# Kernel optimization log

Measured on AMD Instinct MI355X. Metric: run time of the kernel, lower is better.

## Reference

```python
import jax, jax.numpy as jnp
import numpy as np

N_NODES = 50000
N_EDGES = 300000
F_IN = 11
D = 256


def _gcn_conv(h, src, dst, deg_inv_sqrt, W, b, n):
    """PyG GCNConv: out = D^{-1/2} (A + I) D^{-1/2} (h W) + b.
    src/dst already include self-loops; deg_inv_sqrt precomputed."""
    norm = deg_inv_sqrt[src] * deg_inv_sqrt[dst]          # [E+N]
    hw = h @ W                                            # [N, D]
    msg = hw[src] * norm[:, None]                         # [E+N, D]
    out = jax.ops.segment_sum(msg, dst, num_segments=n)   # [N, D]
    return out + b


def setup_inputs() -> dict:
    key = jax.random.key(0)
    ks = jax.random.split(key, 8)
    x = jax.random.normal(ks[0], (N_NODES, F_IN), dtype=jnp.float32)
    edge_index = jax.random.randint(ks[1], (2, N_EDGES), 0, N_NODES, dtype=jnp.int32)
    s = 0.05
    W_embed = jax.random.normal(ks[2], (F_IN, D), dtype=jnp.float32) * s
    b_embed = jnp.zeros((D,), dtype=jnp.float32)
    W1 = jax.random.normal(ks[3], (D, D), dtype=jnp.float32) * s
    b1 = jnp.zeros((D,), dtype=jnp.float32)
    W2 = jax.random.normal(ks[4], (D, D), dtype=jnp.float32) * s
    b2 = jnp.zeros((D,), dtype=jnp.float32)
    return {"x": x, "edge_index": edge_index, "W_embed": W_embed, "b_embed": b_embed,
            "W1": W1, "b1": b1, "W2": W2, "b2": b2}


def reference(x, edge_index, W_embed, b_embed, W1, b1, W2, b2):
    n = x.shape[0]
    # add self-loops (PyG GCNConv default add_self_loops=True)
    loop = jnp.arange(n, dtype=edge_index.dtype)
    src = jnp.concatenate([edge_index[0], loop])
    dst = jnp.concatenate([edge_index[1], loop])
    # symmetric normalization: deg over target index with unit edge weights
    deg = jax.ops.segment_sum(jnp.ones(src.shape, dtype=x.dtype), dst, num_segments=n)
    deg_inv_sqrt = jnp.where(deg > 0, jax.lax.rsqrt(jnp.maximum(deg, 1e-12)), 0.0)

    h = jax.nn.relu(x @ W_embed + b_embed)                # embed + relu
    h = jax.nn.relu(_gcn_conv(h, src, dst, deg_inv_sqrt, W1, b1, n))
    h = _gcn_conv(h, src, dst, deg_inv_sqrt, W2, b2, n)
    return h
```

## Files before the change

kernel.cpp:

```cpp
#include <hip/hip_runtime.h>

#define N_NODES 50000
#define N_EDGES 300000
#define N_TOT   350000
#define D       256
#define MPAD    50048
#define SCAN_B  196

typedef __attribute__((ext_vector_type(8))) short bf16x8;
typedef __attribute__((ext_vector_type(4))) float f32x4;
typedef __attribute__((ext_vector_type(8))) unsigned short u16x8;

__device__ __forceinline__ float bf2f(unsigned short b) {
    union { unsigned u; float f; } v; v.u = ((unsigned)b) << 16; return v.f;
}
__device__ __forceinline__ unsigned short f2bf(float f) {
    union { float f; unsigned u; } v; v.f = f;
    unsigned u = v.u;
    unsigned r = (u + 0x7FFFu + ((u >> 16) & 1u)) >> 16;
    return (unsigned short)r;
}
__device__ __forceinline__ void g2lds16(const unsigned short* g, unsigned short* l) {
    __builtin_amdgcn_global_load_lds(
        (const __attribute__((address_space(1))) void*)g,
        (__attribute__((address_space(3))) void*)l, 16, 0, 0);
}

__global__ __launch_bounds__(256) void k1_kernel(
        const float* __restrict__ x, const int* __restrict__ ei,
        const float* __restrict__ We, const float* __restrict__ be,
        const float* __restrict__ W1, const float* __restrict__ W2,
        int* __restrict__ cnt,
        unsigned short* __restrict__ Wt1, unsigned short* __restrict__ Wt2,
        unsigned short* __restrict__ hA) {
    int t = threadIdx.x, b = blockIdx.x;
    int tid = b * 256 + t;

    if (tid < N_TOT) {
        int dst = (tid < N_EDGES) ? ei[N_EDGES + tid] : (tid - N_EDGES);
        atomicAdd(&cnt[dst], 1);
    }
    if (tid < 2 * D * D) {
        int wsel = tid >> 16, rem = tid & 65535;
        int tt = rem >> 8, bb = rem & 255;
        const float* W = wsel ? W2 : W1;
        unsigned short* Wt = wsel ? Wt2 : Wt1;
        Wt[bb * D + tt] = f2bf(W[tt * D + bb]);
    }
    float w[11];
    #pragma unroll
    for (int k = 0; k < 11; ++k) w[k] = We[k * D + t];
    float bb = be[t];
    #pragma unroll
    for (int ni = 0; ni < 8; ++ni) {
        int node = b * 8 + ni;
        float acc = 0.f;
        if (node < N_NODES) {
            acc = bb;
            #pragma unroll
            for (int k = 0; k < 11; ++k) acc += x[node * 11 + k] * w[k];
            acc = fmaxf(acc, 0.f);
        }
        hA[(size_t)node * D + t] = f2bf(acc);
    }
}

__global__ __launch_bounds__(256) void k2_kernel(const int* __restrict__ cnt,
                                                 float* __restrict__ dis,
                                                 int* __restrict__ locs,
                                                 int* __restrict__ bsum,
                                                 int* __restrict__ done) {
    __shared__ int ws[4];
    __shared__ int amLast;
    int t = threadIdx.x, lane = t & 63, wv = t >> 6;
    int i = blockIdx.x * 256 + t;
    int v = (i < N_NODES) ? cnt[i] : 0;
    if (i < N_NODES) dis[i] = rsqrtf((float)v);
    int s = v;
    #pragma unroll
    for (int d = 1; d < 64; d <<= 1) {
        int u = __shfl_up(s, d, 64);
        if (lane >= d) s += u;
    }
    if (lane == 63) ws[wv] = s;
    __syncthreads();
    int off = 0;
    #pragma unroll
    for (int k = 0; k < 4; ++k) if (k < wv) off += ws[k];
    s += off;
    if (i < N_NODES) locs[i] = s;

    if (t == 255) {
        bsum[blockIdx.x] = s;
        __threadfence();
        amLast = (atomicAdd(done, 1) == SCAN_B - 1);
    }
    __syncthreads();
    if (amLast) {
        __threadfence();
        int vv = 0;
        if (t < SCAN_B)
            vv = __hip_atomic_load(&bsum[t], __ATOMIC_RELAXED, __HIP_MEMORY_SCOPE_AGENT);
        int ss = vv;
        #pragma unroll
        for (int d = 1; d < 64; d <<= 1) {
            int u = __shfl_up(ss, d, 64);
            if (lane >= d) ss += u;
        }
        __syncthreads();
        if (lane == 63) ws[wv] = ss;
        __syncthreads();
        int off2 = 0;
        #pragma unroll
        for (int k = 0; k < 4; ++k) if (k < wv) off2 += ws[k];
        ss += off2;
        if (t < SCAN_B) bsum[t] = ss - vv;
    }
}

__global__ void k3_kernel(const int* __restrict__ ei, const int* __restrict__ locs,
                          const int* __restrict__ bsum, int* __restrict__ fc,
                          int* __restrict__ rowptr, int* __restrict__ esrc) {
    int tid = blockIdx.x * 256 + threadIdx.x;
    if (tid == 0) rowptr[0] = 0;
    if (tid < N_NODES)
        rowptr[tid + 1] = locs[tid] + bsum[tid >> 8];
    if (tid < N_TOT) {
        int src, dst;
        if (tid < N_EDGES) { src = ei[tid]; dst = ei[N_EDGES + tid]; }
        else               { src = dst = tid - N_EDGES; }
        int base = bsum[dst >> 8] + ((dst & 255) ? locs[dst - 1] : 0);
        int pos = base + atomicAdd(&fc[dst], 1);
        esrc[pos] = src;
    }
}

__global__ __launch_bounds__(256) void gemm_kernel(const unsigned short* __restrict__ A,
                                                   const unsigned short* __restrict__ Bt,
                                                   unsigned short* __restrict__ C) {
    __shared__ unsigned short lA[128 * 32];
    __shared__ unsigned short lB[128 * 32];
    int t = threadIdx.x;
    int wv = t >> 6, lane = t & 63;
    int m0 = blockIdx.x * 128;
    int n0 = blockIdx.y * 128;
    int moff = (wv & 1) * 64, noff = (wv >> 1) * 64;
    int q = lane >> 4, r = lane & 15;

    int srow = t >> 2;
    int skof = (t & 3) * 8;

    const unsigned short* Ag0 = A  + (size_t)(m0 + srow) * D + skof;
    const unsigned short* Ag1 = Ag0 + (size_t)64 * D;
    const unsigned short* Bg0 = Bt + (size_t)(n0 + srow) * D + skof;
    const unsigned short* Bg1 = Bg0 + (size_t)64 * D;
    unsigned short* lA0 = lA + t * 8;
    unsigned short* lA1 = lA0 + 64 * 32;
    unsigned short* lB0 = lB + t * 8;
    unsigned short* lB1 = lB0 + 64 * 32;

    f32x4 acc[4][4] = {};
    for (int kk = 0; kk < D; kk += 32) {
        __syncthreads();
        g2lds16(Ag0 + kk, lA0);
        g2lds16(Ag1 + kk, lA1);
        g2lds16(Bg0 + kk, lB0);
        g2lds16(Bg1 + kk, lB1);
        __syncthreads();
        bf16x8 a[4], b[4];
        #pragma unroll
        for (int mt = 0; mt < 4; ++mt)
            a[mt] = *(const bf16x8*)(lA + (moff + mt * 16 + r) * 32 + q * 8);
        #pragma unroll
        for (int nt = 0; nt < 4; ++nt)
            b[nt] = *(const bf16x8*)(lB + (noff + nt * 16 + r) * 32 + q * 8);
        #pragma unroll
        for (int mt = 0; mt < 4; ++mt)
            #pragma unroll
            for (int nt = 0; nt < 4; ++nt)
                acc[mt][nt] = __builtin_amdgcn_mfma_f32_16x16x32_bf16(a[mt], b[nt], acc[mt][nt], 0, 0, 0);
    }
    #pragma unroll
    for (int mt = 0; mt < 4; ++mt)
        #pragma unroll
        for (int nt = 0; nt < 4; ++nt) {
            int col  = n0 + noff + nt * 16 + r;
            int rowb = m0 + moff + mt * 16 + q * 4;
            #pragma unroll
            for (int i = 0; i < 4; ++i)
                C[(size_t)(rowb + i) * D + col] = f2bf(acc[mt][nt][i]);
        }
}

__global__ __launch_bounds__(256) void agg_kernel(const unsigned short* __restrict__ hw,
                                                  const int* __restrict__ rowptr,
                                                  const int* __restrict__ esrc,
                                                  const float* __restrict__ dis,
                                                  const float* __restrict__ bias,
                                                  unsigned short* __restrict__ out_bf,
                                                  float* __restrict__ out_f32,
                                                  int mode) {
    int wid  = threadIdx.x >> 6;
    int lane = threadIdx.x & 63;
    int node = blockIdx.x * 4 + wid;
    if (node >= N_NODES) return;
    int s0 = rowptr[node], s1 = rowptr[node + 1];
    int half = lane >> 5, hl = lane & 31;

    float acc[8] = {};
    for (int base = s0; base < s1; base += 64) {
        int ec = s1 - base; if (ec > 64) ec = 64;
        int srcl = 0; float dsl = 0.f;
        if (lane < ec) { srcl = esrc[base + lane]; dsl = dis[srcl]; }
        int it = (ec + 1) >> 1;
        int   sc = __shfl(srcl, half, 64);
        float nc = __shfl(dsl,  half, 64);
        u16x8 hc = *(const u16x8*)(hw + (size_t)sc * D + hl * 8);
        for (int i = 1; i < it; ++i) {
            int   e  = 2 * i + half;
            int   sn = __shfl(srcl, e, 64);
            float nn = __shfl(dsl,  e, 64);
            u16x8 hn = *(const u16x8*)(hw + (size_t)sn * D + hl * 8);
            #pragma unroll
            for (int k = 0; k < 8; ++k) acc[k] += nc * bf2f(hc[k]);
            nc = nn; hc = hn;
        }
        #pragma unroll
        for (int k = 0; k < 8; ++k) acc[k] += nc * bf2f(hc[k]);
    }
    #pragma unroll
    for (int k = 0; k < 8; ++k) acc[k] += __shfl_xor(acc[k], 32, 64);

    if (lane < 32) {
        int c = hl * 8;
        float dn = dis[node];
        float4 bv0 = *(const float4*)(bias + c);
        float4 bv1 = *(const float4*)(bias + c + 4);
        float v[8];
        v[0] = dn * acc[0] + bv0.x; v[1] = dn * acc[1] + bv0.y;
        v[2] = dn * acc[2] + bv0.z; v[3] = dn * acc[3] + bv0.w;
        v[4] = dn * acc[4] + bv1.x; v[5] = dn * acc[5] + bv1.y;
        v[6] = dn * acc[6] + bv1.z; v[7] = dn * acc[7] + bv1.w;
        if (mode) {
            u16x8 ov;
            #pragma unroll
            for (int k = 0; k < 8; ++k) ov[k] = f2bf(fmaxf(v[k], 0.f));
            *(u16x8*)(out_bf + (size_t)node * D + c) = ov;
        } else {
            float4 o0 = { v[0], v[1], v[2], v[3] };
            float4 o1 = { v[4], v[5], v[6], v[7] };
            *(float4*)(out_f32 + (size_t)node * D + c)     = o0;
            *(float4*)(out_f32 + (size_t)node * D + c + 4) = o1;
        }
    }
}

extern "C" void kernel_launch(void* const* d_in, const int* in_sizes, int n_in,
                              void* d_out, int out_size, void* d_ws, size_t ws_size,
                              hipStream_t stream) {
    const float* x  = (const float*)d_in[0];
    const int*   ei = (const int*)d_in[1];
    const float* We = (const float*)d_in[2];
    const float* be = (const float*)d_in[3];
    const float* W1 = (const float*)d_in[4];
    const float* b1 = (const float*)d_in[5];
    const float* W2 = (const float*)d_in[6];
    const float* b2 = (const float*)d_in[7];
    float* out = (float*)d_out;

    char* w = (char*)d_ws;
    auto alloc = [&](size_t bytes) {
        char* p = w;
        w += (bytes + 255) & ~(size_t)255;
        return p;
    };
    int*            cnt    = (int*)alloc((size_t)N_NODES * 4);
    int*            fc     = (int*)alloc((size_t)N_NODES * 4);
    int*            done   = (int*)alloc(4);
    size_t zero_span = (size_t)((char*)(done + 64) - (char*)cnt);
    int*            rowptr = (int*)alloc((size_t)(N_NODES + 1) * 4);
    int*            locs   = (int*)alloc((size_t)N_NODES * 4);
    int*            bsum   = (int*)alloc((size_t)SCAN_B * 4);
    float*          dis    = (float*)alloc((size_t)N_NODES * 4);
    int*            esrc   = (int*)alloc((size_t)N_TOT * 4);
    unsigned short* Wt1    = (unsigned short*)alloc((size_t)D * D * 2);
    unsigned short* Wt2    = (unsigned short*)alloc((size_t)D * D * 2);
    unsigned short* hA     = (unsigned short*)alloc((size_t)MPAD * D * 2);
    unsigned short* hW     = (unsigned short*)alloc((size_t)MPAD * D * 2);

    hipMemsetAsync(cnt, 0, zero_span, stream);
    k1_kernel<<<MPAD / 8, 256, 0, stream>>>(x, ei, We, be, W1, W2, cnt, Wt1, Wt2, hA);
    k2_kernel<<<SCAN_B, 256, 0, stream>>>(cnt, dis, locs, bsum, done);
    k3_kernel<<<(N_TOT + 255) / 256, 256, 0, stream>>>(ei, locs, bsum, fc, rowptr, esrc);

    dim3 ggrid(MPAD / 128, 2);
    gemm_kernel<<<ggrid, 256, 0, stream>>>(hA, Wt1, hW);
    agg_kernel<<<(N_NODES + 3) / 4, 256, 0, stream>>>(hW, rowptr, esrc, dis, b1, hA, nullptr, 1);

    gemm_kernel<<<ggrid, 256, 0, stream>>>(hA, Wt2, hW);
    agg_kernel<<<(N_NODES + 3) / 4, 256, 0, stream>>>(hW, rowptr, esrc, dis, b2, nullptr, out, 0);
}
```

Baseline: 236.0 us.

## Fuse degree scan into first GEMM and precompute per-edge normalization

Moves the degree prefix-scan (k2) into the first GEMM launch as a prologue on the first 196 blocks, removing one kernel launch. k3 now runs after the GEMM and also writes a per-edge norm array (dis[src]*dis[dst]) in CSR order. The aggregation kernels then read the norm contiguously instead of gathering dis[src] and scaling by dis[dst]. This trades an extra 1.4MB array write and read for fewer random gathers. It also adds a prologue with extra syncthreads and LDS in the GEMM blocks.

```diff
diff --git a/kernel.cpp b/kernel.cpp
--- a/kernel.cpp
+++ b/kernel.cpp
@@ -65,62 +65,10 @@
     }
 }
 
-__global__ __launch_bounds__(256) void k2_kernel(const int* __restrict__ cnt,
-                                                 float* __restrict__ dis,
-                                                 int* __restrict__ locs,
-                                                 int* __restrict__ bsum,
-                                                 int* __restrict__ done) {
-    __shared__ int ws[4];
-    __shared__ int amLast;
-    int t = threadIdx.x, lane = t & 63, wv = t >> 6;
-    int i = blockIdx.x * 256 + t;
-    int v = (i < N_NODES) ? cnt[i] : 0;
-    if (i < N_NODES) dis[i] = rsqrtf((float)v);
-    int s = v;
-    #pragma unroll
-    for (int d = 1; d < 64; d <<= 1) {
-        int u = __shfl_up(s, d, 64);
-        if (lane >= d) s += u;
-    }
-    if (lane == 63) ws[wv] = s;
-    __syncthreads();
-    int off = 0;
-    #pragma unroll
-    for (int k = 0; k < 4; ++k) if (k < wv) off += ws[k];
-    s += off;
-    if (i < N_NODES) locs[i] = s;
-
-    if (t == 255) {
-        bsum[blockIdx.x] = s;
-        __threadfence();
-        amLast = (atomicAdd(done, 1) == SCAN_B - 1);
-    }
-    __syncthreads();
-    if (amLast) {
-        __threadfence();
-        int vv = 0;
-        if (t < SCAN_B)
-            vv = __hip_atomic_load(&bsum[t], __ATOMIC_RELAXED, __HIP_MEMORY_SCOPE_AGENT);
-        int ss = vv;
-        #pragma unroll
-        for (int d = 1; d < 64; d <<= 1) {
-            int u = __shfl_up(ss, d, 64);
-            if (lane >= d) ss += u;
-        }
-        __syncthreads();
-        if (lane == 63) ws[wv] = ss;
-        __syncthreads();
-        int off2 = 0;
-        #pragma unroll
-        for (int k = 0; k < 4; ++k) if (k < wv) off2 += ws[k];
-        ss += off2;
-        if (t < SCAN_B) bsum[t] = ss - vv;
-    }
-}
-
 __global__ void k3_kernel(const int* __restrict__ ei, const int* __restrict__ locs,
-                          const int* __restrict__ bsum, int* __restrict__ fc,
-                          int* __restrict__ rowptr, int* __restrict__ esrc) {
+                          const int* __restrict__ bsum, const float* __restrict__ dis,
+                          int* __restrict__ fc, int* __restrict__ rowptr,
+                          int* __restrict__ esrc, float* __restrict__ enorm) {
     int tid = blockIdx.x * 256 + threadIdx.x;
     if (tid == 0) rowptr[0] = 0;
     if (tid < N_NODES)
@@ -131,16 +79,72 @@
         else               { src = dst = tid - N_EDGES; }
         int base = bsum[dst >> 8] + ((dst & 255) ? locs[dst - 1] : 0);
         int pos = base + atomicAdd(&fc[dst], 1);
-        esrc[pos] = src;
+        esrc[pos]  = src;
+        enorm[pos] = dis[src] * dis[dst];
     }
 }
 
 __global__ __launch_bounds__(256) void gemm_kernel(const unsigned short* __restrict__ A,
                                                    const unsigned short* __restrict__ Bt,
-                                                   unsigned short* __restrict__ C) {
+                                                   unsigned short* __restrict__ C,
+                                                   const int* __restrict__ cnt,
+                                                   float* __restrict__ dis,
+                                                   int* __restrict__ locs,
+                                                   int* __restrict__ bsum,
+                                                   int* __restrict__ done) {
     __shared__ unsigned short lA[128 * 32];
     __shared__ unsigned short lB[128 * 32];
+    __shared__ int ws[4];
+    __shared__ int amLast;
     int t = threadIdx.x;
+
+    if (cnt && blockIdx.y == 0 && blockIdx.x < SCAN_B) {
+        int lane = t & 63, wv4 = t >> 6;
+        int i = blockIdx.x * 256 + t;
+        int v = (i < N_NODES) ? cnt[i] : 0;
+        if (i < N_NODES) dis[i] = rsqrtf((float)v);
+        int s = v;
+        #pragma unroll
+        for (int d = 1; d < 64; d <<= 1) {
+            int u = __shfl_up(s, d, 64);
+            if (lane >= d) s += u;
+        }
+        if (lane == 63) ws[wv4] = s;
+        __syncthreads();
+        int off = 0;
+        #pragma unroll
+        for (int k = 0; k < 4; ++k) if (k < wv4) off += ws[k];
+        s += off;
+        if (i < N_NODES) locs[i] = s;
+        if (t == 255) {
+            bsum[blockIdx.x] = s;
+            __threadfence();
+            amLast = (atomicAdd(done, 1) == SCAN_B - 1);
+        }
+        __syncthreads();
+        if (amLast) {
+            __threadfence();
+            int vv = 0;
+            if (t < SCAN_B)
+                vv = __hip_atomic_load(&bsum[t], __ATOMIC_RELAXED, __HIP_MEMORY_SCOPE_AGENT);
+            int ss = vv;
+            #pragma unroll
+            for (int d = 1; d < 64; d <<= 1) {
+                int u = __shfl_up(ss, d, 64);
+                if (lane >= d) ss += u;
+            }
+            __syncthreads();
+            if (lane == 63) ws[wv4] = ss;
+            __syncthreads();
+            int off2 = 0;
+            #pragma unroll
+            for (int k = 0; k < 4; ++k) if (k < wv4) off2 += ws[k];
+            ss += off2;
+            if (t < SCAN_B) bsum[t] = ss - vv;
+        }
+        __syncthreads();
+    }
+
     int wv = t >> 6, lane = t & 63;
     int m0 = blockIdx.x * 128;
     int n0 = blockIdx.y * 128;
@@ -195,7 +199,7 @@
 __global__ __launch_bounds__(256) void agg_kernel(const unsigned short* __restrict__ hw,
                                                   const int* __restrict__ rowptr,
                                                   const int* __restrict__ esrc,
-                                                  const float* __restrict__ dis,
+                                                  const float* __restrict__ enorm,
                                                   const float* __restrict__ bias,
                                                   unsigned short* __restrict__ out_bf,
                                                   float* __restrict__ out_f32,
@@ -210,16 +214,16 @@
     float acc[8] = {};
     for (int base = s0; base < s1; base += 64) {
         int ec = s1 - base; if (ec > 64) ec = 64;
-        int srcl = 0; float dsl = 0.f;
-        if (lane < ec) { srcl = esrc[base + lane]; dsl = dis[srcl]; }
+        int srcl = 0; float nml = 0.f;
+        if (lane < ec) { srcl = esrc[base + lane]; nml = enorm[base + lane]; }
         int it = (ec + 1) >> 1;
         int   sc = __shfl(srcl, half, 64);
-        float nc = __shfl(dsl,  half, 64);
+        float nc = __shfl(nml,  half, 64);
         u16x8 hc = *(const u16x8*)(hw + (size_t)sc * D + hl * 8);
         for (int i = 1; i < it; ++i) {
             int   e  = 2 * i + half;
             int   sn = __shfl(srcl, e, 64);
-            float nn = __shfl(dsl,  e, 64);
+            float nn = __shfl(nml,  e, 64);
             u16x8 hn = *(const u16x8*)(hw + (size_t)sn * D + hl * 8);
             #pragma unroll
             for (int k = 0; k < 8; ++k) acc[k] += nc * bf2f(hc[k]);
@@ -233,14 +237,13 @@
 
     if (lane < 32) {
         int c = hl * 8;
-        float dn = dis[node];
         float4 bv0 = *(const float4*)(bias + c);
         float4 bv1 = *(const float4*)(bias + c + 4);
         float v[8];
-        v[0] = dn * acc[0] + bv0.x; v[1] = dn * acc[1] + bv0.y;
-        v[2] = dn * acc[2] + bv0.z; v[3] = dn * acc[3] + bv0.w;
-        v[4] = dn * acc[4] + bv1.x; v[5] = dn * acc[5] + bv1.y;
-        v[6] = dn * acc[6] + bv1.z; v[7] = dn * acc[7] + bv1.w;
+        v[0] = acc[0] + bv0.x; v[1] = acc[1] + bv0.y;
+        v[2] = acc[2] + bv0.z; v[3] = acc[3] + bv0.w;
+        v[4] = acc[4] + bv1.x; v[5] = acc[5] + bv1.y;
+        v[6] = acc[6] + bv1.z; v[7] = acc[7] + bv1.w;
         if (mode) {
             u16x8 ov;
             #pragma unroll
@@ -283,6 +286,7 @@
     int*            bsum   = (int*)alloc((size_t)SCAN_B * 4);
     float*          dis    = (float*)alloc((size_t)N_NODES * 4);
     int*            esrc   = (int*)alloc((size_t)N_TOT * 4);
+    float*          enorm  = (float*)alloc((size_t)N_TOT * 4);
     unsigned short* Wt1    = (unsigned short*)alloc((size_t)D * D * 2);
     unsigned short* Wt2    = (unsigned short*)alloc((size_t)D * D * 2);
     unsigned short* hA     = (unsigned short*)alloc((size_t)MPAD * D * 2);
@@ -290,13 +294,16 @@
 
     hipMemsetAsync(cnt, 0, zero_span, stream);
     k1_kernel<<<MPAD / 8, 256, 0, stream>>>(x, ei, We, be, W1, W2, cnt, Wt1, Wt2, hA);
-    k2_kernel<<<SCAN_B, 256, 0, stream>>>(cnt, dis, locs, bsum, done);
-    k3_kernel<<<(N_TOT + 255) / 256, 256, 0, stream>>>(ei, locs, bsum, fc, rowptr, esrc);
 
     dim3 ggrid(MPAD / 128, 2);
-    gemm_kernel<<<ggrid, 256, 0, stream>>>(hA, Wt1, hW);
-    agg_kernel<<<(N_NODES + 3) / 4, 256, 0, stream>>>(hW, rowptr, esrc, dis, b1, hA, nullptr, 1);
-
-    gemm_kernel<<<ggrid, 256, 0, stream>>>(hA, Wt2, hW);
-    agg_kernel<<<(N_NODES + 3) / 4, 256, 0, stream>>>(hW, rowptr, esrc, dis, b2, nullptr, out, 0);
-}
+    gemm_kernel<<<ggrid, 256, 0, stream>>>(hA, Wt1, hW, cnt, dis, locs, bsum, done);
+    k3_kernel<<<(N_TOT + 255) / 256, 256, 0, stream>>>(ei, locs, bsum, dis, fc,
+                                                       rowptr, esrc, enorm);
+    agg_kernel<<<(N_NODES + 3) / 4, 256, 0, stream>>>(hW, rowptr, esrc, enorm, b1,
+                                                      hA, nullptr, 1);
+
+    gemm_kernel<<<ggrid, 256, 0, stream>>>(hA, Wt2, hW, nullptr, nullptr, nullptr,
+                                           nullptr, nullptr);
+    agg_kernel<<<(N_NODES + 3) / 4, 256, 0, stream>>>(hW, rowptr, esrc, enorm, b2,
+                                                      nullptr, out, 0);
+}
```

Result: no change. 234.2 us (-0.8%).
